# Performance work log

Hardware: AMD Instinct MI355X
Metric: run time of the kernel (lower is better)

The kernel has to match this reference:

```python
import jax, jax.numpy as jnp
import numpy as np

DIM = 2048
N_HEADS = 32
N_KV_HEADS = 8
HEAD_DIM = DIM // N_HEADS
N_REP = N_HEADS // N_KV_HEADS
BSZ, SEQ = 2, 2048


def setup_inputs() -> dict:
    key = jax.random.key(0)
    ks = jax.random.split(key, 6)
    hidden_states = jax.random.normal(ks[0], (BSZ, SEQ, DIM), jnp.float32)
    # additive causal mask [1,1,S,S]
    causal = jnp.tril(jnp.ones((SEQ, SEQ), jnp.bool_))
    attention_mask = jnp.where(causal, 0.0, -1e9).astype(jnp.float32)[None, None]
    # RoPE tables [S, head_dim]
    inv_freq = 1.0 / (10000.0 ** (np.arange(0, HEAD_DIM, 2, dtype=np.float32) / HEAD_DIM))
    t = np.arange(SEQ, dtype=np.float32)
    freqs = np.outer(t, inv_freq)  # [S, head_dim/2]
    emb = np.concatenate([freqs, freqs], axis=-1)  # [S, head_dim]
    position_cos = jnp.asarray(np.cos(emb), jnp.float32)
    position_sin = jnp.asarray(np.sin(emb), jnp.float32)
    s = 0.02
    Wq = jax.random.normal(ks[1], (DIM, DIM), jnp.float32) * s
    Wk = jax.random.normal(ks[2], (N_KV_HEADS * HEAD_DIM, DIM), jnp.float32) * s
    Wv = jax.random.normal(ks[3], (N_KV_HEADS * HEAD_DIM, DIM), jnp.float32) * s
    Wo = jax.random.normal(ks[4], (DIM, DIM), jnp.float32) * s
    return {"hidden_states": hidden_states, "attention_mask": attention_mask,
            "position_cos": position_cos, "position_sin": position_sin,
            "Wq": Wq, "Wk": Wk, "Wv": Wv, "Wo": Wo}


def _rotate_half(x):
    x1, x2 = jnp.split(x, 2, axis=-1)
    return jnp.concatenate([-x2, x1], axis=-1)


def _apply_rope(x, cos, sin):
    # x: [b, h, s, d]; cos/sin: [s, d] broadcast over (b, h)
    return x * cos + _rotate_half(x) * sin


def reference(hidden_states, attention_mask, position_cos, position_sin, Wq, Wk, Wv, Wo):
    b, s, _ = hidden_states.shape
    q = jnp.einsum('bsd,ed->bse', hidden_states, Wq).reshape(b, s, N_HEADS, HEAD_DIM).transpose(0, 2, 1, 3)
    k = jnp.einsum('bsd,ed->bse', hidden_states, Wk).reshape(b, s, N_KV_HEADS, HEAD_DIM).transpose(0, 2, 1, 3)
    v = jnp.einsum('bsd,ed->bse', hidden_states, Wv).reshape(b, s, N_KV_HEADS, HEAD_DIM).transpose(0, 2, 1, 3)
    q = _apply_rope(q, position_cos, position_sin)
    k = _apply_rope(k, position_cos, position_sin)
    # GQA: group query heads over kv heads instead of physically repeating k/v
    qg = q.reshape(b, N_KV_HEADS, N_REP, s, HEAD_DIM)
    scores = jnp.einsum('bgrqd,bgkd->bgrqk', qg, k) * (1.0 / jnp.sqrt(jnp.float32(HEAD_DIM)))
    scores = scores + attention_mask[:, :, None, :s, :s]
    weights = jax.nn.softmax(scores.astype(jnp.float32), axis=-1).astype(q.dtype)
    attn = jnp.einsum('bgrqk,bgkd->bgrqd', weights, v)
    attn = attn.reshape(b, N_HEADS, s, HEAD_DIM).transpose(0, 2, 1, 3).reshape(b, s, DIM)
    out = jnp.einsum('bsd,ed->bse', attn, Wo)
    return out
```

## Files before the change

### kernel.cpp

```cpp
#include <hip/hip_runtime.h>
#include <math.h>

#define BSZ 2
#define SEQ 2048
#define DIM 2048
#define NH 32
#define NKV 8
#define HD 64
#define KVDIM 512

typedef short short8 __attribute__((ext_vector_type(8)));
typedef short short4v __attribute__((ext_vector_type(4)));
typedef float f32x4 __attribute__((ext_vector_type(4)));
typedef int i32x4 __attribute__((ext_vector_type(4)));

__device__ __forceinline__ short fbf(float x) {
    unsigned u = __float_as_uint(x);
    u = (u + 0x7fffu + ((u >> 16) & 1u)) >> 16;
    return (short)u;
}

#define AS1(p) ((const __attribute__((address_space(1))) void*)(p))
#define AS3(p) ((__attribute__((address_space(3))) void*)(p))

#if defined(__has_builtin)
#if __has_builtin(__builtin_amdgcn_permlane16_swap) && __has_builtin(__builtin_amdgcn_permlane32_swap)
#define HAVE_PERMLANE 1
#endif
#endif

__device__ __forceinline__ float redmax4(float x) {
#ifdef HAVE_PERMLANE
    {
        auto p = __builtin_amdgcn_permlane16_swap(__float_as_uint(x), __float_as_uint(x), false, false);
        x = fmaxf(__uint_as_float(p[0]), __uint_as_float(p[1]));
    }
    {
        auto p = __builtin_amdgcn_permlane32_swap(__float_as_uint(x), __float_as_uint(x), false, false);
        x = fmaxf(__uint_as_float(p[0]), __uint_as_float(p[1]));
    }
#else
    x = fmaxf(x, __shfl_xor(x, 16));
    x = fmaxf(x, __shfl_xor(x, 32));
#endif
    return x;
}
__device__ __forceinline__ float redsum4(float x) {
#ifdef HAVE_PERMLANE
    {
        auto p = __builtin_amdgcn_permlane16_swap(__float_as_uint(x), __float_as_uint(x), false, false);
        x = __uint_as_float(p[0]) + __uint_as_float(p[1]);
    }
    {
        auto p = __builtin_amdgcn_permlane32_swap(__float_as_uint(x), __float_as_uint(x), false, false);
        x = __uint_as_float(p[0]) + __uint_as_float(p[1]);
    }
#else
    x += __shfl_xor(x, 16);
    x += __shfl_xor(x, 32);
#endif
    return x;
}

__global__ __launch_bounds__(256) void prep(const float* __restrict__ X,
                                            const float* __restrict__ Wq,
                                            const float* __restrict__ Wk,
                                            const float* __restrict__ Wv,
                                            const float* __restrict__ Wo,
                                            short* __restrict__ Xb,
                                            short* __restrict__ Wqkv,
                                            short* __restrict__ Wob) {
    int i = blockIdx.x * 256 + threadIdx.x;
    const float* src; short* dst; int j;
    if (i < 2097152)      { src = X;  dst = Xb;             j = i; }
    else if (i < 3145728) { src = Wq; dst = Wqkv;           j = i - 2097152; }
    else if (i < 3407872) { src = Wk; dst = Wqkv + 4194304; j = i - 3145728; }
    else if (i < 3670016) { src = Wv; dst = Wqkv + 5242880; j = i - 3407872; }
    else                  { src = Wo; dst = Wob;            j = i - 3670016; }
    float4 f = ((const float4*)src)[j];
    short4v s = { fbf(f.x), fbf(f.y), fbf(f.z), fbf(f.w) };
    ((short4v*)dst)[j] = s;
}

__global__ __launch_bounds__(512, 2) void gemm_qkv(const short* __restrict__ A,
                                                   const short* __restrict__ W,
                                                   const float* __restrict__ cosT,
                                                   const float* __restrict__ sinT,
                                                   short* __restrict__ Qo,
                                                   short* __restrict__ Ko,
                                                   short* __restrict__ Vo) {
    __shared__ short SM[65536];
    const int K = 2048;
    const int NT = 64;
    const int tid = threadIdx.x;
    const int lane = tid & 63, wave = tid >> 6;
    const int l15 = lane & 15, quad = lane >> 4;
    const int wm = (wave >> 2) * 128;
    const int wn = (wave & 3) * 64;
    const int orig = blockIdx.x;
    const int wgid = (orig & 7) * 24 + (orig >> 3);
    const int by = wgid / 12, bx = wgid - by * 12;
    const int m0 = by * 256, n0 = bx * 256;

    size_t aoff[2], boff[2]; int lslot[2];
#pragma unroll
    for (int v = 0; v < 2; ++v) {
        int s = v * 512 + tid;
        int pr = s >> 3, w = s & 7;
        int row = (pr << 1) | (w & 1);
        int c = (w >> 1) ^ (pr & 3);
        aoff[v] = (size_t)(m0 + row) * K + c * 8;
        boff[v] = (size_t)(n0 + row) * K + c * 8;
        lslot[v] = s * 8;
    }
    const int r0a = wm + l15;
    const int pa = r0a >> 1;
    const int slotA0 = pa * 8 + (((quad ^ (pa & 3)) << 1) | (r0a & 1));
    const int r0b = wn + l15;
    const int pb = r0b >> 1;
    const int slotB0 = pb * 8 + (((quad ^ (pb & 3)) << 1) | (r0b & 1));

    f32x4 acc[8][4] = {};

    auto issue = [&](int t) {
        const int kb = t * 32;
        short* Ad = SM + (t & 3) * 8192;
        short* Bd = SM + 32768 + (t & 3) * 8192;
#pragma unroll
        for (int v = 0; v < 2; ++v) {
            __builtin_amdgcn_global_load_lds(AS1(A + aoff[v] + kb), AS3(Ad + lslot[v]), 16, 0, 0);
            __builtin_amdgcn_global_load_lds(AS1(W + boff[v] + kb), AS3(Bd + lslot[v]), 16, 0, 0);
        }
    };
    issue(0); issue(1); issue(2);
    asm volatile("s_waitcnt vmcnt(8)" ::: "memory");
    __builtin_amdgcn_s_barrier();
    asm volatile("" ::: "memory");
    __builtin_amdgcn_sched_barrier(0);

    for (int t = 0; t < NT; ++t) {
        if (t < NT - 3) issue(t + 3);
        const short* Ab = SM + (t & 3) * 8192;
        const short* Bb = SM + 32768 + (t & 3) * 8192;
        short8 af[8], bf8[4];
#pragma unroll
        for (int j = 0; j < 4; ++j)
            bf8[j] = *(const short8*)&Bb[(slotB0 + j * 64) * 8];
#pragma unroll
        for (int i = 0; i < 8; ++i)
            af[i] = *(const short8*)&Ab[(slotA0 + i * 64) * 8];
        __builtin_amdgcn_s_setprio(1);
#pragma unroll
        for (int i = 0; i < 8; ++i)
#pragma unroll
            for (int j = 0; j < 4; ++j)
                acc[i][j] = __builtin_amdgcn_mfma_f32_16x16x32_bf16(af[i], bf8[j], acc[i][j], 0, 0, 0);
        __builtin_amdgcn_s_setprio(0);
        if (t < NT - 3)       asm volatile("s_waitcnt vmcnt(8)" ::: "memory");
        else if (t == NT - 3) asm volatile("s_waitcnt vmcnt(4)" ::: "memory");
        else if (t == NT - 2) asm volatile("s_waitcnt vmcnt(0)" ::: "memory");
        __builtin_amdgcn_s_barrier();
        asm volatile("" ::: "memory");
        __builtin_amdgcn_sched_barrier(0);
    }

    const int n0r = n0 + wn;
    if (n0r < 2560) {
        short* dst; int heads, hh; float scale;
        if (n0r < 2048) { dst = Qo; heads = NH;  hh = n0r >> 6;          scale = 0.125f * 1.44269504088896f; }
        else            { dst = Ko; heads = NKV; hh = (n0r - 2048) >> 6; scale = 1.0f; }
        short* EB = SM + wave * 8192;
#pragma unroll
        for (int i = 0; i < 8; ++i)
#pragma unroll
            for (int r = 0; r < 4; ++r) {
                int rr = i * 16 + quad * 4 + r;
                int s = (m0 + wm + rr) & (SEQ - 1);
                int msk = ((rr >> 1) & 7) * 8;
#pragma unroll
                for (int jp = 0; jp < 2; ++jp) {
                    int d1 = jp * 16 + l15;
                    float c1 = cosT[s * HD + d1], s1v = sinT[s * HD + d1];
                    float x1 = acc[i][jp][r], x2 = acc[i][jp + 2][r];
                    EB[rr * 64 + (d1 ^ msk)]        = fbf((x1 * c1 - x2 * s1v) * scale);
                    EB[rr * 64 + ((d1 + 32) ^ msk)] = fbf((x2 * c1 + x1 * s1v) * scale);
                }
            }
#pragma unroll
        for (int t = 0; t < 16; ++t) {
            int rr = (lane >> 3) + t * 8;
            int c = lane & 7;
            short8 v8 = *(const short8*)&EB[rr * 64 + c * 8];
            int dchunk = c ^ ((rr >> 1) & 7);
            int mrow = m0 + wm + rr;
            int s = mrow & (SEQ - 1), bb = mrow >> 11;
            *(short8*)&dst[((size_t)(bb * SEQ + s) * heads + hh) * HD + dchunk * 8] = v8;
        }
    } else {
        const int hh = (n0r - 2560) >> 6;
#pragma unroll
        for (int i = 0; i < 8; ++i) {
            int mrow4 = m0 + wm + i * 16 + quad * 4;
            int s_abs = mrow4 & (SEQ - 1);
            int bb = mrow4 >> 11;
            int blk = s_abs >> 6, kk = s_abs & 63;
            int ob = ((kk >> 5) << 3) | (((kk >> 2) & 3) << 1) | ((kk >> 4) & 1);
#pragma unroll
            for (int j = 0; j < 4; ++j) {
                int d = j * 16 + l15;
                short4v pk = { fbf(acc[i][j][0]), fbf(acc[i][j][1]),
                               fbf(acc[i][j][2]), fbf(acc[i][j][3]) };
                *(short4v*)&Vo[(((size_t)(bb * NKV + hh) * HD + d) * SEQ) + blk * 64 + ob * 4] = pk;
            }
        }
    }
}

__global__ __launch_bounds__(512, 2) void gemm_bf16(const short* __restrict__ A,
                                                    const short* __restrict__ W,
                                                    float* __restrict__ C,
                                                    int M, int N, int K) {
    __shared__ short SM[49152];
    const int NT = K >> 5;
    const int tid = threadIdx.x;
    const int lane = tid & 63, wave = tid >> 6;
    const int l15 = lane & 15, quad = lane >> 4;
    const int wm = (wave >> 1) * 64;
    const int wn = (wave & 1) * 64;
    const int orig = blockIdx.x;
    const int wgid = (orig & 7) * 32 + (orig >> 3);
    const int by = wgid >> 4, bx = wgid & 15;
    const int m0 = by * 256, n0 = bx * 128;

    size_t aoff[2]; int lslotA[2];
#pragma unroll
    for (int v = 0; v < 2; ++v) {
        int s = v * 512 + tid;
        int pr = s >> 3, w = s & 7;
        int row = (pr << 1) | (w & 1);
        int c = (w >> 1) ^ (pr & 3);
        aoff[v] = (size_t)(m0 + row) * K + c * 8;
        lslotA[v] = s * 8;
    }
    size_t boff; int lslotB;
    {
        int s = tid;
        int pr = s >> 3, w = s & 7;
        int row = (pr << 1) | (w & 1);
        int c = (w >> 1) ^ (pr & 3);
        boff = (size_t)(n0 + row) * K + c * 8;
        lslotB = s * 8;
    }
    const int r0a = wm + l15;
    const int pa = r0a >> 1;
    const int slotA0 = pa * 8 + (((quad ^ (pa & 3)) << 1) | (r0a & 1));
    const int r0b = wn + l15;
    const int pb = r0b >> 1;
    const int slotB0 = pb * 8 + (((quad ^ (pb & 3)) << 1) | (r0b & 1));

    f32x4 acc[4][4] = {};

    auto issue = [&](int t) {
        const int kb = t * 32;
        short* Ad = SM + (t & 3) * 8192;
        short* Bd = SM + 32768 + (t & 3) * 4096;
#pragma unroll
        for (int v = 0; v < 2; ++v)
            __builtin_amdgcn_global_load_lds(AS1(A + aoff[v] + kb), AS3(Ad + lslotA[v]), 16, 0, 0);
        __builtin_amdgcn_global_load_lds(AS1(W + boff + kb), AS3(Bd + lslotB), 16, 0, 0);
    };
    issue(0); issue(1); issue(2);
    asm volatile("s_waitcnt vmcnt(6)" ::: "memory");
    __builtin_amdgcn_s_barrier();
    asm volatile("" ::: "memory");
    __builtin_amdgcn_sched_barrier(0);

    for (int t = 0; t < NT; ++t) {
        if (t < NT - 3) issue(t + 3);
        const short* Ab = SM + (t & 3) * 8192;
        const short* Bb = SM + 32768 + (t & 3) * 4096;
        short8 af[4], bf8[4];
#pragma unroll
        for (int j = 0; j < 4; ++j)
            bf8[j] = *(const short8*)&Bb[(slotB0 + j * 64) * 8];
#pragma unroll
        for (int i = 0; i < 4; ++i)
            af[i] = *(const short8*)&Ab[(slotA0 + i * 64) * 8];
        __builtin_amdgcn_s_setprio(1);
#pragma unroll
        for (int i = 0; i < 4; ++i)
#pragma unroll
            for (int j = 0; j < 4; ++j)
                acc[i][j] = __builtin_amdgcn_mfma_f32_16x16x32_bf16(af[i], bf8[j], acc[i][j], 0, 0, 0);
        __builtin_amdgcn_s_setprio(0);
        if (t < NT - 3)       asm volatile("s_waitcnt vmcnt(6)" ::: "memory");
        else if (t == NT - 3) asm volatile("s_waitcnt vmcnt(3)" ::: "memory");
        else if (t == NT - 2) asm volatile("s_waitcnt vmcnt(0)" ::: "memory");
        __builtin_amdgcn_s_barrier();
        asm volatile("" ::: "memory");
        __builtin_amdgcn_sched_barrier(0);
    }
#pragma unroll
    for (int i = 0; i < 4; ++i)
#pragma unroll
        for (int j = 0; j < 4; ++j)
#pragma unroll
            for (int r = 0; r < 4; ++r)
                C[(size_t)(m0 + wm + i * 16 + quad * 4 + r) * N + n0 + wn + j * 16 + l15] = acc[i][j][r];
}

__global__ __launch_bounds__(512, 4) void flash4(const short* __restrict__ Qb,
                                                 const short* __restrict__ Kb,
                                                 const short* __restrict__ VT,
                                                 short* __restrict__ O) {
    __shared__ short Ks[2][64 * 64];
    __shared__ short Vs[2][64 * 64];
    const int d = blockIdx.x;
    const int bh = (d & 511) >> 3;
    const int qt = (d < 512) ? 15 - (d & 7) : (d & 7);
    const int b = bh >> 5, h = bh & 31, kvh = h >> 2;
    const int tid = threadIdx.x;
    const int wave = tid >> 6, lane = tid & 63;
    const int l15 = lane & 15, quad = lane >> 4;

    const short* qp = Qb + ((size_t)b * SEQ + qt * 128 + wave * 16 + l15) * DIM + h * HD + quad * 8;
    short8 qf0 = *(const short8*)qp;
    short8 qf1 = *(const short8*)(qp + 32);

    f32x4 o[4] = {};
    float m = -1e30f, l = 0.f;

    const short* Kbase = Kb + (size_t)b * SEQ * KVDIM + kvh * HD;
    const short* Vbase = VT + (size_t)(b * NKV + kvh) * HD * SEQ;

    const int srow = tid >> 3;
    const int scol = ((tid & 7) ^ (srow & 7)) * 8;
    auto issue = [&](int kt, int bi) {
        __builtin_amdgcn_global_load_lds(AS1(Kbase + (size_t)(kt * 64 + srow) * KVDIM + scol),
                                         AS3(&Ks[bi][tid * 8]), 16, 0, 0);
        __builtin_amdgcn_global_load_lds(AS1(Vbase + (size_t)srow * SEQ + kt * 64 + scol),
                                         AS3(&Vs[bi][tid * 8]), 16, 0, 0);
    };
    issue(0, 0);
    const int nkt = 2 * qt + 2;
    const int qmin = qt * 128 + wave * 16;
    for (int kt = 0; kt < nkt; ++kt) {
        const int bi = kt & 1;
        __builtin_amdgcn_s_barrier();
        asm volatile("" ::: "memory");
        if (kt + 1 < nkt) {
            issue(kt + 1, bi ^ 1);
            asm volatile("s_waitcnt vmcnt(2)" ::: "memory");
        } else {
            asm volatile("s_waitcnt vmcnt(0)" ::: "memory");
        }
        __builtin_amdgcn_sched_barrier(0);
        if (kt * 64 > qmin + 15) continue;

        f32x4 st[4] = {};
        __builtin_amdgcn_s_setprio(1);
#pragma unroll
        for (int kh = 0; kh < 2; ++kh) {
            const int cs = ((kh * 4 + quad) ^ (l15 & 7)) * 8;
#pragma unroll
            for (int nt = 0; nt < 4; ++nt) {
                short8 ka = *(const short8*)&Ks[bi][(nt * 16 + l15) * 64 + cs];
                st[nt] = __builtin_amdgcn_mfma_f32_16x16x32_bf16(ka, kh ? qf1 : qf0, st[nt], 0, 0, 0);
            }
        }
        __builtin_amdgcn_s_setprio(0);
        if (kt * 64 + 63 > qmin) {
            const int q = qmin + l15;
#pragma unroll
            for (int nt = 0; nt < 4; ++nt)
                if (kt * 64 + nt * 16 + 15 > qmin) {
#pragma unroll
                    for (int r = 0; r < 4; ++r)
                        if (kt * 64 + nt * 16 + quad * 4 + r > q) st[nt][r] = -1e30f;
                }
        }
        float mnt[4];
#pragma unroll
        for (int nt = 0; nt < 4; ++nt)
            mnt[nt] = fmaxf(fmaxf(fmaxf(st[nt][0], st[nt][1]), st[nt][2]), st[nt][3]);
        float mx = redmax4(fmaxf(fmaxf(mnt[0], mnt[1]), fmaxf(mnt[2], mnt[3])));

        const bool noskip = !__all(mx <= m);
        float mn = m;
        float al = 1.0f;
        float alr[4];
        if (noskip) {
            mn = fmaxf(m, mx);
            al = __builtin_amdgcn_exp2f(m - mn);
            m = mn;
#pragma unroll
            for (int r = 0; r < 4; ++r) alr[r] = __shfl(al, quad * 4 + r);
        }
        i32x4 aw[2];
        f32x4 rs4 = {};
#pragma unroll
        for (int nt = 0; nt < 4; ++nt) {
            f32x4 pv;
#pragma unroll
            for (int r = 0; r < 4; ++r) pv[r] = __builtin_amdgcn_exp2f(st[nt][r] - mn);
            rs4 += pv;
            unsigned u0 = __float_as_uint(pv[0]) + 0x8000u;
            unsigned u1 = __float_as_uint(pv[1]) + 0x8000u;
            unsigned u2 = __float_as_uint(pv[2]) + 0x8000u;
            unsigned u3 = __float_as_uint(pv[3]) + 0x8000u;
            aw[nt >> 1][(nt & 1) * 2 + 0] = (int)__builtin_amdgcn_perm(u1, u0, 0x07060302u);
            aw[nt >> 1][(nt & 1) * 2 + 1] = (int)__builtin_amdgcn_perm(u3, u2, 0x07060302u);
        }
        float rs = redsum4((rs4[0] + rs4[1]) + (rs4[2] + rs4[3]));
        l = l * al + rs;
        if (noskip) {
#pragma unroll
            for (int dt = 0; dt < 4; ++dt) {
                o[dt][0] *= alr[0]; o[dt][1] *= alr[1];
                o[dt][2] *= alr[2]; o[dt][3] *= alr[3];
            }
        }
        __builtin_amdgcn_s_setprio(1);
#pragma unroll
        for (int dt = 0; dt < 4; ++dt) {
            f32x4 t = o[dt];
#pragma unroll
            for (int kh = 0; kh < 2; ++kh) {
                const int slot = (kh * 4 + quad) ^ (l15 & 7);
                short8 vf = *(const short8*)&Vs[bi][(dt * 16 + l15) * 64 + slot * 8];
                t = __builtin_amdgcn_mfma_f32_16x16x32_bf16(__builtin_bit_cast(short8, aw[kh]), vf, t, 0, 0, 0);
            }
            o[dt] = t;
        }
        __builtin_amdgcn_s_setprio(0);
    }
    float li = 1.0f / l;
    float lr[4];
#pragma unroll
    for (int r = 0; r < 4; ++r) lr[r] = __shfl(li, quad * 4 + r);
    short* Oo = O + ((size_t)b * SEQ + qt * 128 + wave * 16 + quad * 4) * DIM + h * HD + l15;
#pragma unroll
    for (int r = 0; r < 4; ++r)
#pragma unroll
        for (int dt = 0; dt < 4; ++dt)
            Oo[(size_t)r * DIM + dt * 16] = fbf(o[dt][r] * lr[r]);
}

extern "C" void kernel_launch(void* const* d_in, const int* in_sizes, int n_in,
                              void* d_out, int out_size, void* d_ws, size_t ws_size,
                              hipStream_t stream) {
    const float* X    = (const float*)d_in[0];
    const float* cosT = (const float*)d_in[2];
    const float* sinT = (const float*)d_in[3];
    const float* Wq   = (const float*)d_in[4];
    const float* Wk   = (const float*)d_in[5];
    const float* Wv   = (const float*)d_in[6];
    const float* Wo   = (const float*)d_in[7];

    char* ws = (char*)d_ws;
    short* Xb    = (short*)(ws);
    short* ATTb  = Xb;
    short* WQKVb = (short*)(ws + 16777216);
    short* Wob   = (short*)(ws + 29360128);
    short* Qbb   = (short*)(ws + 37748736);
    short* Kbb   = (short*)(ws + 54525952);
    short* VTb   = (short*)(ws + 58720256);

    const int M = BSZ * SEQ;

    prep<<<dim3(18432), dim3(256), 0, stream>>>(X, Wq, Wk, Wv, Wo, Xb, WQKVb, Wob);
    gemm_qkv<<<dim3(192), dim3(512), 0, stream>>>(Xb, WQKVb, cosT, sinT, Qbb, Kbb, VTb);
    flash4<<<dim3(1024), dim3(512), 0, stream>>>(Qbb, Kbb, VTb, ATTb);
    gemm_bf16<<<dim3(256), dim3(512), 0, stream>>>(ATTb, Wob, (float*)d_out, M, DIM, DIM);
}
```

Before: 291.1 us.

## Restructure QKV GEMM main loop into 64-wide K tiles with staggered half-tile prefetch

The QKV projection GEMM moves from a 4-stage ring of 32-wide K slices to a double-buffered 64-wide K tile layout with an XOR swizzle per row. Each iteration splits into four MFMA phases, and the global-to-LDS loads for the next tiles are placed between them in quarter chunks. This interleaves memory traffic with compute and halves the number of outer iterations. In exchange it adds more barriers per iteration and leaves less prefetch depth, which could expose load latency.

```diff
diff --git a/kernel.cpp b/kernel.cpp
--- a/kernel.cpp
+++ b/kernel.cpp
@@ -91,7 +91,7 @@
                                                    short* __restrict__ Vo) {
     __shared__ short SM[65536];
     const int K = 2048;
-    const int NT = 64;
+    const int NT = 32;
     const int tid = threadIdx.x;
     const int lane = tid & 63, wave = tid >> 6;
     const int l15 = lane & 15, quad = lane >> 4;
@@ -102,63 +102,129 @@
     const int by = wgid / 12, bx = wgid - by * 12;
     const int m0 = by * 256, n0 = bx * 256;
 
-    size_t aoff[2], boff[2]; int lslot[2];
+    const int cs0 = (quad ^ (l15 & 7)) * 8;
+    const int cs1 = ((4 + quad) ^ (l15 & 7)) * 8;
+    const int halfA = wm >> 7;
+    const int halfB = wn >> 7;
+    const int rB0 = wn & 127;
+
+    int srow[2], spc[2];
 #pragma unroll
     for (int v = 0; v < 2; ++v) {
         int s = v * 512 + tid;
-        int pr = s >> 3, w = s & 7;
-        int row = (pr << 1) | (w & 1);
-        int c = (w >> 1) ^ (pr & 3);
-        aoff[v] = (size_t)(m0 + row) * K + c * 8;
-        boff[v] = (size_t)(n0 + row) * K + c * 8;
-        lslot[v] = s * 8;
-    }
-    const int r0a = wm + l15;
-    const int pa = r0a >> 1;
-    const int slotA0 = pa * 8 + (((quad ^ (pa & 3)) << 1) | (r0a & 1));
-    const int r0b = wn + l15;
-    const int pb = r0b >> 1;
-    const int slotB0 = pb * 8 + (((quad ^ (pb & 3)) << 1) | (r0b & 1));
+        srow[v] = s >> 3;
+        spc[v] = ((s & 7) ^ ((s >> 3) & 7)) * 8;
+    }
 
     f32x4 acc[8][4] = {};
 
-    auto issue = [&](int t) {
-        const int kb = t * 32;
-        short* Ad = SM + (t & 3) * 8192;
-        short* Bd = SM + 32768 + (t & 3) * 8192;
-#pragma unroll
-        for (int v = 0; v < 2; ++v) {
-            __builtin_amdgcn_global_load_lds(AS1(A + aoff[v] + kb), AS3(Ad + lslot[v]), 16, 0, 0);
-            __builtin_amdgcn_global_load_lds(AS1(W + boff[v] + kb), AS3(Bd + lslot[v]), 16, 0, 0);
-        }
+    auto stg = [&](int arr, int bbuf, int half, int kt2) {
+        const short* gs = arr ? W : A;
+        const int row0 = (arr ? n0 : m0) + half * 128;
+        short* db = SM + arr * 32768 + bbuf * 16384 + half * 8192;
+#pragma unroll
+        for (int v = 0; v < 2; ++v)
+            __builtin_amdgcn_global_load_lds(AS1(gs + (size_t)(row0 + srow[v]) * K + kt2 * 64 + spc[v]),
+                                             AS3(db + (v * 512 + tid) * 8), 16, 0, 0);
     };
-    issue(0); issue(1); issue(2);
-    asm volatile("s_waitcnt vmcnt(8)" ::: "memory");
+
+    stg(1, 0, 0, 0); stg(1, 0, 1, 0); stg(0, 0, 0, 0); stg(0, 0, 1, 0);
+    stg(1, 1, 0, 1); stg(1, 1, 1, 1); stg(0, 1, 0, 1);
+    asm volatile("s_waitcnt vmcnt(6)" ::: "memory");
     __builtin_amdgcn_s_barrier();
     asm volatile("" ::: "memory");
     __builtin_amdgcn_sched_barrier(0);
 
-    for (int t = 0; t < NT; ++t) {
-        if (t < NT - 3) issue(t + 3);
-        const short* Ab = SM + (t & 3) * 8192;
-        const short* Bb = SM + 32768 + (t & 3) * 8192;
-        short8 af[8], bf8[4];
-#pragma unroll
-        for (int j = 0; j < 4; ++j)
-            bf8[j] = *(const short8*)&Bb[(slotB0 + j * 64) * 8];
-#pragma unroll
-        for (int i = 0; i < 8; ++i)
-            af[i] = *(const short8*)&Ab[(slotA0 + i * 64) * 8];
-        __builtin_amdgcn_s_setprio(1);
-#pragma unroll
-        for (int i = 0; i < 8; ++i)
-#pragma unroll
-            for (int j = 0; j < 4; ++j)
-                acc[i][j] = __builtin_amdgcn_mfma_f32_16x16x32_bf16(af[i], bf8[j], acc[i][j], 0, 0, 0);
-        __builtin_amdgcn_s_setprio(0);
-        if (t < NT - 3)       asm volatile("s_waitcnt vmcnt(8)" ::: "memory");
-        else if (t == NT - 3) asm volatile("s_waitcnt vmcnt(4)" ::: "memory");
-        else if (t == NT - 2) asm volatile("s_waitcnt vmcnt(0)" ::: "memory");
+    for (int kt = 0; kt < NT; ++kt) {
+        const int b = kt & 1;
+        const short* Ab = SM + b * 16384 + halfA * 8192;
+        const short* Bb = SM + 32768 + b * 16384 + halfB * 8192;
+        short8 bf_r[4][2], af_r[4][2];
+
+#pragma unroll
+        for (int j = 0; j < 4; ++j) {
+            const short* p = &Bb[(rB0 + j * 16 + l15) * 64];
+            bf_r[j][0] = *(const short8*)(p + cs0);
+            bf_r[j][1] = *(const short8*)(p + cs1);
+        }
+#pragma unroll
+        for (int i = 0; i < 4; ++i) {
+            const short* p = &Ab[(i * 16 + l15) * 64];
+            af_r[i][0] = *(const short8*)(p + cs0);
+            af_r[i][1] = *(const short8*)(p + cs1);
+        }
+        if (kt + 1 < NT) stg(0, (kt + 1) & 1, 1, kt + 1);
+        __builtin_amdgcn_s_barrier();
+        asm volatile("" ::: "memory");
+        __builtin_amdgcn_sched_barrier(0);
+        __builtin_amdgcn_s_setprio(1);
+#pragma unroll
+        for (int i = 0; i < 4; ++i)
+#pragma unroll
+            for (int j = 0; j < 2; ++j) {
+                acc[i][j] = __builtin_amdgcn_mfma_f32_16x16x32_bf16(af_r[i][0], bf_r[j][0], acc[i][j], 0, 0, 0);
+                acc[i][j] = __builtin_amdgcn_mfma_f32_16x16x32_bf16(af_r[i][1], bf_r[j][1], acc[i][j], 0, 0, 0);
+            }
+        __builtin_amdgcn_s_setprio(0);
+        __builtin_amdgcn_s_barrier();
+        asm volatile("" ::: "memory");
+        __builtin_amdgcn_sched_barrier(0);
+
+        if (kt + 2 < NT) stg(1, b, 0, kt + 2);
+        __builtin_amdgcn_s_barrier();
+        asm volatile("" ::: "memory");
+        __builtin_amdgcn_sched_barrier(0);
+        __builtin_amdgcn_s_setprio(1);
+#pragma unroll
+        for (int i = 0; i < 4; ++i)
+#pragma unroll
+            for (int j = 2; j < 4; ++j) {
+                acc[i][j] = __builtin_amdgcn_mfma_f32_16x16x32_bf16(af_r[i][0], bf_r[j][0], acc[i][j], 0, 0, 0);
+                acc[i][j] = __builtin_amdgcn_mfma_f32_16x16x32_bf16(af_r[i][1], bf_r[j][1], acc[i][j], 0, 0, 0);
+            }
+        __builtin_amdgcn_s_setprio(0);
+        __builtin_amdgcn_s_barrier();
+        asm volatile("" ::: "memory");
+        __builtin_amdgcn_sched_barrier(0);
+
+#pragma unroll
+        for (int i = 0; i < 4; ++i) {
+            const short* p = &Ab[((i + 4) * 16 + l15) * 64];
+            af_r[i][0] = *(const short8*)(p + cs0);
+            af_r[i][1] = *(const short8*)(p + cs1);
+        }
+        if (kt + 2 < NT) stg(1, b, 1, kt + 2);
+        __builtin_amdgcn_s_barrier();
+        asm volatile("" ::: "memory");
+        __builtin_amdgcn_sched_barrier(0);
+        __builtin_amdgcn_s_setprio(1);
+#pragma unroll
+        for (int i = 0; i < 4; ++i)
+#pragma unroll
+            for (int j = 0; j < 2; ++j) {
+                acc[i + 4][j] = __builtin_amdgcn_mfma_f32_16x16x32_bf16(af_r[i][0], bf_r[j][0], acc[i + 4][j], 0, 0, 0);
+                acc[i + 4][j] = __builtin_amdgcn_mfma_f32_16x16x32_bf16(af_r[i][1], bf_r[j][1], acc[i + 4][j], 0, 0, 0);
+            }
+        __builtin_amdgcn_s_setprio(0);
+        __builtin_amdgcn_s_barrier();
+        asm volatile("" ::: "memory");
+        __builtin_amdgcn_sched_barrier(0);
+
+        if (kt + 2 < NT) stg(0, b, 0, kt + 2);
+        if (kt < NT - 2)       asm volatile("s_waitcnt vmcnt(6)" ::: "memory");
+        else if (kt == NT - 2) asm volatile("s_waitcnt vmcnt(0)" ::: "memory");
+        __builtin_amdgcn_s_barrier();
+        asm volatile("" ::: "memory");
+        __builtin_amdgcn_sched_barrier(0);
+        __builtin_amdgcn_s_setprio(1);
+#pragma unroll
+        for (int i = 0; i < 4; ++i)
+#pragma unroll
+            for (int j = 2; j < 4; ++j) {
+                acc[i + 4][j] = __builtin_amdgcn_mfma_f32_16x16x32_bf16(af_r[i][0], bf_r[j][0], acc[i + 4][j], 0, 0, 0);
+                acc[i + 4][j] = __builtin_amdgcn_mfma_f32_16x16x32_bf16(af_r[i][1], bf_r[j][1], acc[i + 4][j], 0, 0, 0);
+            }
+        __builtin_amdgcn_s_setprio(0);
         __builtin_amdgcn_s_barrier();
         asm volatile("" ::: "memory");
         __builtin_amdgcn_sched_barrier(0);
```

Measured after the change: 291.1 us. Within noise of the previous version (+0.0%).

## Shrink QKV GEMM tile to 256x128 with 3-stage pipeline for more blocks

Applied to the files above, without the earlier changes.

Changes the QKV projection GEMM from 256x256 tiles (192 blocks) to 256x128 tiles (384 blocks). Each wave now computes 64x64 instead of 128x64. The LDS ring drops from 4 stages to 3 to cut shared memory, and launch bounds are raised to request 4 blocks per CU. The aim is to fill all CUs on the MI355X, since 192 blocks underfill the device. The cost is lower arithmetic intensity per tile, more A-matrix reloads, and a shallower prefetch pipeline.

```diff
diff --git a/kernel.cpp b/kernel.cpp
--- a/kernel.cpp
+++ b/kernel.cpp
@@ -82,27 +82,27 @@
     ((short4v*)dst)[j] = s;
 }
 
-__global__ __launch_bounds__(512, 2) void gemm_qkv(const short* __restrict__ A,
+__global__ __launch_bounds__(512, 4) void gemm_qkv(const short* __restrict__ A,
                                                    const short* __restrict__ W,
                                                    const float* __restrict__ cosT,
                                                    const float* __restrict__ sinT,
                                                    short* __restrict__ Qo,
                                                    short* __restrict__ Ko,
                                                    short* __restrict__ Vo) {
-    __shared__ short SM[65536];
+    __shared__ short SM[36864];
     const int K = 2048;
     const int NT = 64;
     const int tid = threadIdx.x;
     const int lane = tid & 63, wave = tid >> 6;
     const int l15 = lane & 15, quad = lane >> 4;
-    const int wm = (wave >> 2) * 128;
-    const int wn = (wave & 3) * 64;
+    const int wm = (wave >> 1) * 64;
+    const int wn = (wave & 1) * 64;
     const int orig = blockIdx.x;
-    const int wgid = (orig & 7) * 24 + (orig >> 3);
-    const int by = wgid / 12, bx = wgid - by * 12;
-    const int m0 = by * 256, n0 = bx * 256;
-
-    size_t aoff[2], boff[2]; int lslot[2];
+    const int wgid = (orig & 7) * 48 + (orig >> 3);
+    const int by = wgid / 24, bx = wgid - by * 24;
+    const int m0 = by * 256, n0 = bx * 128;
+
+    size_t aoff[2]; int lslotA[2];
 #pragma unroll
     for (int v = 0; v < 2; ++v) {
         int s = v * 512 + tid;
@@ -110,8 +110,16 @@
         int row = (pr << 1) | (w & 1);
         int c = (w >> 1) ^ (pr & 3);
         aoff[v] = (size_t)(m0 + row) * K + c * 8;
-        boff[v] = (size_t)(n0 + row) * K + c * 8;
-        lslot[v] = s * 8;
+        lslotA[v] = s * 8;
+    }
+    size_t boff; int lslotB;
+    {
+        int s = tid;
+        int pr = s >> 3, w = s & 7;
+        int row = (pr << 1) | (w & 1);
+        int c = (w >> 1) ^ (pr & 3);
+        boff = (size_t)(n0 + row) * K + c * 8;
+        lslotB = s * 8;
     }
     const int r0a = wm + l15;
     const int pa = r0a >> 1;
@@ -120,44 +128,42 @@
     const int pb = r0b >> 1;
     const int slotB0 = pb * 8 + (((quad ^ (pb & 3)) << 1) | (r0b & 1));
 
-    f32x4 acc[8][4] = {};
+    f32x4 acc[4][4] = {};
 
     auto issue = [&](int t) {
         const int kb = t * 32;
-        short* Ad = SM + (t & 3) * 8192;
-        short* Bd = SM + 32768 + (t & 3) * 8192;
-#pragma unroll
-        for (int v = 0; v < 2; ++v) {
-            __builtin_amdgcn_global_load_lds(AS1(A + aoff[v] + kb), AS3(Ad + lslot[v]), 16, 0, 0);
-            __builtin_amdgcn_global_load_lds(AS1(W + boff[v] + kb), AS3(Bd + lslot[v]), 16, 0, 0);
-        }
+        short* Ad = SM + (t % 3) * 8192;
+        short* Bd = SM + 24576 + (t % 3) * 4096;
+#pragma unroll
+        for (int v = 0; v < 2; ++v)
+            __builtin_amdgcn_global_load_lds(AS1(A + aoff[v] + kb), AS3(Ad + lslotA[v]), 16, 0, 0);
+        __builtin_amdgcn_global_load_lds(AS1(W + boff + kb), AS3(Bd + lslotB), 16, 0, 0);
     };
-    issue(0); issue(1); issue(2);
-    asm volatile("s_waitcnt vmcnt(8)" ::: "memory");
+    issue(0); issue(1);
+    asm volatile("s_waitcnt vmcnt(3)" ::: "memory");
     __builtin_amdgcn_s_barrier();
     asm volatile("" ::: "memory");
     __builtin_amdgcn_sched_barrier(0);
 
     for (int t = 0; t < NT; ++t) {
-        if (t < NT - 3) issue(t + 3);
-        const short* Ab = SM + (t & 3) * 8192;
-        const short* Bb = SM + 32768 + (t & 3) * 8192;
-        short8 af[8], bf8[4];
+        if (t + 2 < NT) issue(t + 2);
+        const short* Ab = SM + (t % 3) * 8192;
+        const short* Bb = SM + 24576 + (t % 3) * 4096;
+        short8 af[4], bf8[4];
 #pragma unroll
         for (int j = 0; j < 4; ++j)
             bf8[j] = *(const short8*)&Bb[(slotB0 + j * 64) * 8];
 #pragma unroll
-        for (int i = 0; i < 8; ++i)
+        for (int i = 0; i < 4; ++i)
             af[i] = *(const short8*)&Ab[(slotA0 + i * 64) * 8];
         __builtin_amdgcn_s_setprio(1);
 #pragma unroll
-        for (int i = 0; i < 8; ++i)
+        for (int i = 0; i < 4; ++i)
 #pragma unroll
             for (int j = 0; j < 4; ++j)
                 acc[i][j] = __builtin_amdgcn_mfma_f32_16x16x32_bf16(af[i], bf8[j], acc[i][j], 0, 0, 0);
         __builtin_amdgcn_s_setprio(0);
-        if (t < NT - 3)       asm volatile("s_waitcnt vmcnt(8)" ::: "memory");
-        else if (t == NT - 3) asm volatile("s_waitcnt vmcnt(4)" ::: "memory");
+        if (t < NT - 2)       asm volatile("s_waitcnt vmcnt(3)" ::: "memory");
         else if (t == NT - 2) asm volatile("s_waitcnt vmcnt(0)" ::: "memory");
         __builtin_amdgcn_s_barrier();
         asm volatile("" ::: "memory");
@@ -169,9 +175,9 @@
         short* dst; int heads, hh; float scale;
         if (n0r < 2048) { dst = Qo; heads = NH;  hh = n0r >> 6;          scale = 0.125f * 1.44269504088896f; }
         else            { dst = Ko; heads = NKV; hh = (n0r - 2048) >> 6; scale = 1.0f; }
-        short* EB = SM + wave * 8192;
-#pragma unroll
-        for (int i = 0; i < 8; ++i)
+        short* EB = SM + wave * 4096;
+#pragma unroll
+        for (int i = 0; i < 4; ++i)
 #pragma unroll
             for (int r = 0; r < 4; ++r) {
                 int rr = i * 16 + quad * 4 + r;
@@ -187,7 +193,7 @@
                 }
             }
 #pragma unroll
-        for (int t = 0; t < 16; ++t) {
+        for (int t = 0; t < 8; ++t) {
             int rr = (lane >> 3) + t * 8;
             int c = lane & 7;
             short8 v8 = *(const short8*)&EB[rr * 64 + c * 8];
@@ -199,7 +205,7 @@
     } else {
         const int hh = (n0r - 2560) >> 6;
 #pragma unroll
-        for (int i = 0; i < 8; ++i) {
+        for (int i = 0; i < 4; ++i) {
             int mrow4 = m0 + wm + i * 16 + quad * 4;
             int s_abs = mrow4 & (SEQ - 1);
             int bb = mrow4 >> 11;
@@ -469,7 +475,7 @@
     const int M = BSZ * SEQ;
 
     prep<<<dim3(18432), dim3(256), 0, stream>>>(X, Wq, Wk, Wv, Wo, Xb, WQKVb, Wob);
-    gemm_qkv<<<dim3(192), dim3(512), 0, stream>>>(Xb, WQKVb, cosT, sinT, Qbb, Kbb, VTb);
+    gemm_qkv<<<dim3(384), dim3(512), 0, stream>>>(Xb, WQKVb, cosT, sinT, Qbb, Kbb, VTb);
     flash4<<<dim3(1024), dim3(512), 0, stream>>>(Qbb, Kbb, VTb, ATTb);
     gemm_bf16<<<dim3(256), dim3(512), 0, stream>>>(ATTb, Wob, (float*)d_out, M, DIM, DIM);
 }
```

New measurement: 295.1 us (median of 2 runs). About the same (+1.4%).
